# Kernel tuning notes

Hardware: AMD Instinct MI355X
Metric: run time of the kernel (lower is better)

Reference implementation:

```python
import jax, jax.numpy as jnp
import numpy as np

N = 20000      # nodes
E = 320000     # edges (avg degree 16)
DIN, H1, H2, DOUT = 256, 256, 128, 64


def _lin_params(key, din, dout):
    kw, kb = jax.random.split(key)
    s = 1.0 / np.sqrt(din)
    W = jax.random.uniform(kw, (din, dout), jnp.float32, -s, s)
    b = jax.random.uniform(kb, (dout,), jnp.float32, -s, s)
    return W, b


def setup_inputs() -> dict:
    key = jax.random.key(0)
    keys = jax.random.split(key, 20)
    inp = {
        'x': jax.random.normal(keys[0], (N, DIN), jnp.float32),
        'edge_index': jax.random.randint(keys[1], (2, E), 0, N, jnp.int64),
    }
    dims = [(DIN, H1), (DIN, H1), (DIN, H1),   # layer1 key/query/value
            (H1, H2), (H1, H2), (H1, H2),      # layer2
            (H2, DOUT), (H2, DOUT), (H2, DOUT)]  # layer3
    names = ['k1', 'q1', 'v1', 'k2', 'q2', 'v2', 'k3', 'q3', 'v3']
    for i, (nm, (di, do)) in enumerate(zip(names, dims)):
        W, b = _lin_params(keys[2 + i], di, do)
        inp[nm + '_w'] = W
        inp[nm + '_b'] = b
    # skip (root) weights, no bias per PyG, plus per-conv output bias
    for j, (di, do) in enumerate([(DIN, H1), (H1, H2), (H2, DOUT)], start=1):
        s = 1.0 / np.sqrt(di)
        inp[f's{j}_w'] = jax.random.uniform(keys[11 + 2 * j], (di, do), jnp.float32, -s, s)
        inp[f'bias{j}'] = jnp.zeros((do,), jnp.float32)
    return inp


def _res_gated_conv(x, src, dst, kw, kb, qw, qb, vw, vb, sw, bias):
    # PyG ResGatedGraphConv (flow source_to_target, aggr='add', act=Sigmoid):
    # out_i = lin_skip(x_i) + sum_{j->i} sigmoid(lin_key(x_i) + lin_query(x_j)) * lin_value(x_j) + bias
    k = x @ kw + kb            # [N, D]
    q = x @ qw + qb
    v = x @ vw + vb
    eta = jax.nn.sigmoid(k[dst] + q[src])   # [E, D] edge gate
    msg = eta * v[src]                      # [E, D]
    agg = jax.ops.segment_sum(msg, dst, num_segments=N)  # scatter-add to targets
    return x @ sw + agg + bias


def reference(x, edge_index,
              k1_w, k1_b, q1_w, q1_b, v1_w, v1_b,
              k2_w, k2_b, q2_w, q2_b, v2_w, v2_b,
              k3_w, k3_b, q3_w, q3_b, v3_w, v3_b,
              s1_w, bias1, s2_w, bias2, s3_w, bias3):
    src, dst = edge_index[0], edge_index[1]
    h = _res_gated_conv(x, src, dst, k1_w, k1_b, q1_w, q1_b, v1_w, v1_b, s1_w, bias1)
    # dropout (eval mode -> identity)
    h = _res_gated_conv(h, src, dst, k2_w, k2_b, q2_w, q2_b, v2_w, v2_b, s2_w, bias2)
    h = _res_gated_conv(h, src, dst, k3_w, k3_b, q3_w, q3_b, v3_w, v3_b, s3_w, bias3)
    return jax.nn.softmax(h, axis=1)
```

## Files before the change

### kernel.cpp

```cpp
#include <hip/hip_runtime.h>
#include <hip/hip_bf16.h>
#include <type_traits>


#define NN 20000
#define EE 320000
#define ELLW 64

typedef _Float16 half8 __attribute__((ext_vector_type(8)));
typedef _Float16 half4 __attribute__((ext_vector_type(4)));
typedef _Float16 half2v __attribute__((ext_vector_type(2)));
typedef float f32x4 __attribute__((ext_vector_type(4)));

__device__ __forceinline__ _Float16 f2h(float f) { return (_Float16)f; }
__device__ __forceinline__ float fsigmoid_mul(float v, float x) {
    return v * __builtin_amdgcn_rcpf(1.f + __expf(-x));
}

__global__ void setup_kernel(const int* __restrict__ ei, int* __restrict__ deg,
                             int* __restrict__ flag, int n, int ncheck) {
    const int i = blockIdx.x * blockDim.x + threadIdx.x;
    if (i < n) deg[i] = 0;
    if (blockIdx.x == 0) {
        __shared__ int nz;
        if (threadIdx.x == 0) nz = 0;
        __syncthreads();
        int c = 0;
        for (int t = threadIdx.x; t < ncheck; t += blockDim.x)
            if (ei[2 * t + 1] != 0) c = 1;
        if (c) atomicAdd(&nz, 1);
        __syncthreads();
        if (threadIdx.x == 0) *flag = (nz == 0) ? 1 : 0;
    }
}

__global__ void fill_ell_kernel(const int* __restrict__ ei,
                                const int* __restrict__ i64flag,
                                int* __restrict__ deg, int* __restrict__ col,
                                int E) {
    const int e = blockIdx.x * blockDim.x + threadIdx.x;
    if (e >= E) return;
    int src, dst;
    if (*i64flag) {
        const long long* p = (const long long*)ei;
        src = (int)p[e];
        dst = (int)p[E + e];
    } else {
        src = ei[e];
        dst = ei[E + e];
    }
    const int pos = atomicAdd(&deg[dst], 1);
    if (pos < ELLW) col[dst * ELLW + pos] = src;
}

__global__ void cast_f16_kernel(const float* __restrict__ in,
                                _Float16* __restrict__ out, int n) {
    const int i = (blockIdx.x * blockDim.x + threadIdx.x) * 8;
    if (i >= n) return;
    const float4 f0 = *(const float4*)(in + i);
    const float4 f1 = *(const float4*)(in + i + 4);
    half8 h;
    h[0] = f2h(f0.x); h[1] = f2h(f0.y); h[2] = f2h(f0.z); h[3] = f2h(f0.w);
    h[4] = f2h(f1.x); h[5] = f2h(f1.y); h[6] = f2h(f1.z); h[7] = f2h(f1.w);
    *(half8*)(out + i) = h;
}

struct PrepArgs {
    const float *w[3][4];
    const float *b[3][4];
    _Float16 *wt[3];
    float *cb[3];
};

__global__ void prep_all_kernel(PrepArgs a) {
    const int idx = blockIdx.x * blockDim.x + threadIdx.x;
    int layer, li, K, D, s;
    if (idx < 262144) {
        layer = 0; li = idx; K = 256; D = 256; s = 2;
    } else if (idx < 393216) {
        layer = 1; li = idx - 262144; K = 256; D = 128; s = 1;
    } else if (idx < 425984) {
        layer = 2; li = idx - 393216; K = 128; D = 64; s = 0;
    } else {
        return;
    }
    const int p = li / K;
    const int k = li - p * K;
    const int DV = D >> 6;
    int grp, c;
    if (p < D) {
        grp = 0; c = p;
    } else if (p < 3 * D) {
        const int t = p - D;
        const int g = t >> (s + 1);
        const int r = t & (2 * DV - 1);
        if (r < DV) { grp = 1; c = g * DV + r; }
        else        { grp = 2; c = g * DV + r - DV; }
    } else {
        grp = 3; c = p - 3 * D;
    }
    a.wt[layer][(size_t)p * K + k] = f2h(a.w[layer][grp][(size_t)k * D + c]);
    if (k == 0) a.cb[layer][p] = a.b[layer][grp][c];
}

__global__ __launch_bounds__(256) void gemm_mfma_kernel(
    const _Float16* __restrict__ A, const _Float16* __restrict__ Bt,
    const float* __restrict__ catbias, _Float16* __restrict__ KQV,
    float* __restrict__ Hout, int M, int K, int dshift) {
    __shared__ _Float16 As[2][4096];
    __shared__ _Float16 Bs[2][4096];

    const int D = 1 << dshift;
    const int D3 = 3 * D;
    const int tid = threadIdx.x;
    const int wid = tid >> 6;
    const int lane = tid & 63;
    const int tile_m = blockIdx.x * 128;
    const int tile_n = blockIdx.y * 128;
    const int wm = (wid & 1) * 64;
    const int wn = (wid >> 1) * 64;

    const int st_row = (wid << 4) + (lane >> 2);
    const int st_kc = (lane & 3) << 3;

    auto stage = [&](int buf, int kt) {
#pragma unroll
        for (int j = 0; j < 2; ++j) {
            int ar = tile_m + j * 64 + st_row;
            ar = ar < M ? ar : M - 1;
            const _Float16* ag = A + (size_t)ar * K + kt + st_kc;
            __builtin_amdgcn_global_load_lds(
                (const __attribute__((address_space(1))) unsigned int*)ag,
                (__attribute__((address_space(3))) unsigned int*)
                    &As[buf][j * 2048 + (wid << 9)],
                16, 0, 0);
            const int br = tile_n + j * 64 + st_row;
            const _Float16* bg = Bt + (size_t)br * K + kt + st_kc;
            __builtin_amdgcn_global_load_lds(
                (const __attribute__((address_space(1))) unsigned int*)bg,
                (__attribute__((address_space(3))) unsigned int*)
                    &Bs[buf][j * 2048 + (wid << 9)],
                16, 0, 0);
        }
    };

    stage(0, 0);

    f32x4 acc[4][4] = {};
    const int fr = lane & 15;
    const int fk = (lane >> 4) << 3;
    const int niter = K >> 5;

    for (int it = 0; it < niter; ++it) {
        __syncthreads();
        if (it + 1 < niter) stage((it + 1) & 1, (it + 1) << 5);
        const _Float16* as = As[it & 1];
        const _Float16* bs = Bs[it & 1];
        half8 af[4], bf[4];
#pragma unroll
        for (int mi = 0; mi < 4; ++mi)
            af[mi] = *(const half8*)&as[(wm + mi * 16 + fr) * 32 + fk];
#pragma unroll
        for (int ni = 0; ni < 4; ++ni)
            bf[ni] = *(const half8*)&bs[(wn + ni * 16 + fr) * 32 + fk];
#pragma unroll
        for (int mi = 0; mi < 4; ++mi)
#pragma unroll
            for (int ni = 0; ni < 4; ++ni)
                acc[mi][ni] = __builtin_amdgcn_mfma_f32_16x16x32_f16(
                    af[mi], bf[ni], acc[mi][ni], 0, 0, 0);
    }
    __syncthreads();

    _Float16* zone = &As[0][0] + wid * 2048;
    const int cl = lane & 15;
    const int rq = (lane >> 4) << 2;
    const int col0 = tile_n + wn;
    const int r0 = tile_m + wm;

    if (col0 < D3) {
#pragma unroll
        for (int mi = 0; mi < 4; ++mi) {
#pragma unroll
            for (int ni = 0; ni < 4; ++ni) {
                const float cb = catbias[col0 + ni * 16 + cl];
#pragma unroll
                for (int r = 0; r < 4; ++r)
                    zone[(rq + r) * 72 + ni * 16 + cl] =
                        f2h(acc[mi][ni][r] + cb);
            }
#pragma unroll
            for (int j = 0; j < 2; ++j) {
                const int rr = j * 8 + (lane >> 3);
                const int row = r0 + mi * 16 + rr;
                const half8 v = *(const half8*)&zone[rr * 72 + (lane & 7) * 8];
                if (row < M)
                    *(half8*)&KQV[(size_t)row * D3 + col0 + (lane & 7) * 8] = v;
            }
        }
    } else {
        float* fz = (float*)zone;
        const int cs = col0 - D3;
#pragma unroll
        for (int mi = 0; mi < 4; ++mi) {
#pragma unroll
            for (int ni = 0; ni < 4; ++ni) {
                const float cb = catbias[col0 + ni * 16 + cl];
#pragma unroll
                for (int r = 0; r < 4; ++r)
                    fz[(rq + r) * 64 + ni * 16 + cl] = acc[mi][ni][r] + cb;
            }
#pragma unroll
            for (int j = 0; j < 4; ++j) {
                const int rr = j * 4 + (lane >> 4);
                const int row = r0 + mi * 16 + rr;
                const float4 v = *(const float4*)&fz[rr * 64 + cl * 4];
                if (row < M)
                    *(float4*)&Hout[(size_t)row * D + cs + cl * 4] = v;
            }
        }
    }
}

template <int D, int MODE>
__global__ __launch_bounds__(256) void edge_gather_kernel(
    const int* __restrict__ deg, const int* __restrict__ col,
    const _Float16* __restrict__ KQV, const float* __restrict__ Hskip,
    _Float16* __restrict__ Hh, float* __restrict__ out, int n) {
    constexpr int DV = D / 64;
    constexpr int D3 = 3 * D;
    using qv_t = typename std::conditional<
        DV == 4, half8,
        typename std::conditional<DV == 2, half4, half2v>::type>::type;

    const int node = blockIdx.x * 4 + (threadIdx.x >> 6);
    if (node >= n) return;
    const int lane = threadIdx.x & 63;
    const int ld = lane * DV;

    float k[DV], acc[DV];
    {
        const _Float16* kp = KQV + (size_t)node * D3 + ld;
        if constexpr (DV == 4) {
            const half4 u = *(const half4*)kp;
#pragma unroll
            for (int j = 0; j < 4; ++j) k[j] = (float)u[j];
        } else if constexpr (DV == 2) {
            const half2v u = *(const half2v*)kp;
            k[0] = (float)u[0]; k[1] = (float)u[1];
        } else {
            k[0] = (float)*kp;
        }
    }
#pragma unroll
    for (int j = 0; j < DV; ++j) acc[j] = 0.f;

    int dg = deg[node];
    dg = dg < ELLW ? dg : ELLW;
    const int* cb = col + node * ELLW;

    auto qvload = [&](int src) {
        return *(const qv_t*)(KQV + (size_t)src * D3 + D + 2 * ld);
    };
    auto qvacc = [&](qv_t u) {
#pragma unroll
        for (int j = 0; j < DV; ++j)
            acc[j] += fsigmoid_mul((float)u[DV + j], k[j] + (float)u[j]);
    };

    int e = 0;
    for (; e + 4 <= dg; e += 4) {
        const int s0 = cb[e], s1 = cb[e + 1], s2 = cb[e + 2], s3 = cb[e + 3];
        const qv_t u0 = qvload(s0);
        const qv_t u1 = qvload(s1);
        const qv_t u2 = qvload(s2);
        const qv_t u3 = qvload(s3);
        qvacc(u0); qvacc(u1); qvacc(u2); qvacc(u3);
    }
    for (; e < dg; ++e) qvacc(qvload(cb[e]));

    const float* sp = Hskip + (size_t)node * D + ld;
    float h[DV];
    if constexpr (DV == 4) {
        const float4 s = *(const float4*)sp;
        h[0] = s.x + acc[0]; h[1] = s.y + acc[1];
        h[2] = s.z + acc[2]; h[3] = s.w + acc[3];
    } else if constexpr (DV == 2) {
        const float2 s = *(const float2*)sp;
        h[0] = s.x + acc[0]; h[1] = s.y + acc[1];
    } else {
        h[0] = sp[0] + acc[0];
    }

    if constexpr (MODE == 0) {
        _Float16* op = Hh + (size_t)node * D + ld;
        if constexpr (DV == 4) {
            half4 o;
#pragma unroll
            for (int j = 0; j < 4; ++j) o[j] = f2h(h[j]);
            *(half4*)op = o;
        } else if constexpr (DV == 2) {
            half2v o;
            o[0] = f2h(h[0]); o[1] = f2h(h[1]);
            *(half2v*)op = o;
        } else {
            op[0] = f2h(h[0]);
        }
    } else {
        static_assert(MODE == 0 || DV == 1, "softmax fusion needs D==64");
        float m = h[0];
#pragma unroll
        for (int off = 32; off > 0; off >>= 1)
            m = fmaxf(m, __shfl_xor(m, off, 64));
        const float ex = __expf(h[0] - m);
        float sm = ex;
#pragma unroll
        for (int off = 32; off > 0; off >>= 1) sm += __shfl_xor(sm, off, 64);
        out[(size_t)node * 64 + lane] = ex * __builtin_amdgcn_rcpf(sm);
    }
}

extern "C" void kernel_launch(void* const* d_in, const int* in_sizes, int n_in,
                              void* d_out, int out_size, void* d_ws,
                              size_t ws_size, hipStream_t stream) {
    const float* x = (const float*)d_in[0];
    const int* ei = (const int*)d_in[1];

    char* w = (char*)d_ws;
    _Float16* Xh = (_Float16*)w;              w += (size_t)NN * 256 * 2;
    _Float16* KQV = (_Float16*)w;             w += (size_t)NN * 768 * 2;
    float* Hs = (float*)w;                    w += (size_t)NN * 256 * 4;
    _Float16* H1h = (_Float16*)w;             w += (size_t)NN * 256 * 2;
    _Float16* H2h = (_Float16*)w;             w += (size_t)NN * 128 * 2;
    _Float16* Wt1 = (_Float16*)w;             w += (size_t)1024 * 256 * 2;
    _Float16* Wt2 = (_Float16*)w;             w += (size_t)512 * 256 * 2;
    _Float16* Wt3 = (_Float16*)w;             w += (size_t)256 * 128 * 2;
    float* cb1 = (float*)w;                   w += 1024 * 4;
    float* cb2 = (float*)w;                   w += 512 * 4;
    float* cb3 = (float*)w;                   w += 256 * 4;
    int* i64flag = (int*)w;                   w += 16;
    int* deg = (int*)w;                       w += (size_t)NN * 4;
    int* ell = (int*)w;                       w += (size_t)NN * ELLW * 4;

    const dim3 blk(256);
    const int mblocks = (NN + 127) / 128;
    const int gblocks = (NN + 3) / 4;

    setup_kernel<<<(NN + 255) / 256, blk, 0, stream>>>(ei, deg, i64flag, NN,
                                                       1024);
    fill_ell_kernel<<<(EE + 255) / 256, blk, 0, stream>>>(ei, i64flag, deg,
                                                          ell, EE);

    PrepArgs pa;
    pa.w[0][0] = (const float*)d_in[2];  pa.b[0][0] = (const float*)d_in[3];
    pa.w[0][1] = (const float*)d_in[4];  pa.b[0][1] = (const float*)d_in[5];
    pa.w[0][2] = (const float*)d_in[6];  pa.b[0][2] = (const float*)d_in[7];
    pa.w[1][0] = (const float*)d_in[8];  pa.b[1][0] = (const float*)d_in[9];
    pa.w[1][1] = (const float*)d_in[10]; pa.b[1][1] = (const float*)d_in[11];
    pa.w[1][2] = (const float*)d_in[12]; pa.b[1][2] = (const float*)d_in[13];
    pa.w[2][0] = (const float*)d_in[14]; pa.b[2][0] = (const float*)d_in[15];
    pa.w[2][1] = (const float*)d_in[16]; pa.b[2][1] = (const float*)d_in[17];
    pa.w[2][2] = (const float*)d_in[18]; pa.b[2][2] = (const float*)d_in[19];
    pa.w[0][3] = (const float*)d_in[20]; pa.b[0][3] = (const float*)d_in[21];
    pa.w[1][3] = (const float*)d_in[22]; pa.b[1][3] = (const float*)d_in[23];
    pa.w[2][3] = (const float*)d_in[24]; pa.b[2][3] = (const float*)d_in[25];
    pa.wt[0] = Wt1; pa.wt[1] = Wt2; pa.wt[2] = Wt3;
    pa.cb[0] = cb1; pa.cb[1] = cb2; pa.cb[2] = cb3;
    prep_all_kernel<<<(425984 + 255) / 256, blk, 0, stream>>>(pa);
    cast_f16_kernel<<<(NN * 256 / 8 + 255) / 256, blk, 0, stream>>>(
        x, Xh, NN * 256);

    gemm_mfma_kernel<<<dim3(mblocks, 8), blk, 0, stream>>>(
        Xh, Wt1, cb1, KQV, Hs, NN, 256, 8);
    edge_gather_kernel<256, 0><<<gblocks, blk, 0, stream>>>(
        deg, ell, KQV, Hs, H1h, nullptr, NN);

    gemm_mfma_kernel<<<dim3(mblocks, 4), blk, 0, stream>>>(
        H1h, Wt2, cb2, KQV, Hs, NN, 256, 7);
    edge_gather_kernel<128, 0><<<gblocks, blk, 0, stream>>>(
        deg, ell, KQV, Hs, H2h, nullptr, NN);

    gemm_mfma_kernel<<<dim3(mblocks, 2), blk, 0, stream>>>(
        H2h, Wt3, cb3, KQV, Hs, NN, 128, 6);
    edge_gather_kernel<64, 1><<<gblocks, blk, 0, stream>>>(
        deg, ell, KQV, Hs, nullptr, (float*)d_out, NN);
}
```

Baseline: 283.6 us.

## Fuse setup kernels, overlap ELL fill with first GEMM, store skip in fp16

Merges the degree reset, int64 check, weight prep and input cast into one launch. It also runs the ELL fill as extra blocks of the first GEMM launch, so graph construction overlaps with the matmul. The skip projection is now written as fp16 inside one combined KQVS buffer instead of a separate fp32 array, and the edge gather loads neighbor indices once per wave and broadcasts them by shuffle in batches of 8. This cuts launch count and gather latency, but lowers skip precision and depends on a block-order assumption. The fill blocks write deg and col while the GEMM blocks read nothing from them, so the fusion is safe.

Measured after the change: 262.3 us. 1.08x faster.

```diff
diff --git a/kernel.cpp b/kernel.cpp
--- a/kernel.cpp
+++ b/kernel.cpp
@@ -17,106 +17,84 @@
     return v * __builtin_amdgcn_rcpf(1.f + __expf(-x));
 }
 
-__global__ void setup_kernel(const int* __restrict__ ei, int* __restrict__ deg,
-                             int* __restrict__ flag, int n, int ncheck) {
-    const int i = blockIdx.x * blockDim.x + threadIdx.x;
-    if (i < n) deg[i] = 0;
-    if (blockIdx.x == 0) {
+struct PrepArgs {
+    const float* w[3][4];
+    const float* b[3][4];
+    _Float16* wt[3];
+    float* cb[3];
+};
+
+__global__ __launch_bounds__(256) void setup_all_kernel(
+    const int* __restrict__ ei, int* __restrict__ deg, int* __restrict__ flag,
+    const float* __restrict__ x, _Float16* __restrict__ Xh, PrepArgs a) {
+    const int b = blockIdx.x;
+    const int tid = threadIdx.x;
+    if (b < 79) {
+        const int i = b * 256 + tid;
+        if (i < NN) deg[i] = 0;
+    } else if (b == 79) {
         __shared__ int nz;
-        if (threadIdx.x == 0) nz = 0;
+        if (tid == 0) nz = 0;
         __syncthreads();
         int c = 0;
-        for (int t = threadIdx.x; t < ncheck; t += blockDim.x)
+        for (int t = tid; t < 1024; t += 256)
             if (ei[2 * t + 1] != 0) c = 1;
         if (c) atomicAdd(&nz, 1);
         __syncthreads();
-        if (threadIdx.x == 0) *flag = (nz == 0) ? 1 : 0;
-    }
-}
-
-__global__ void fill_ell_kernel(const int* __restrict__ ei,
-                                const int* __restrict__ i64flag,
-                                int* __restrict__ deg, int* __restrict__ col,
-                                int E) {
-    const int e = blockIdx.x * blockDim.x + threadIdx.x;
-    if (e >= E) return;
-    int src, dst;
-    if (*i64flag) {
-        const long long* p = (const long long*)ei;
-        src = (int)p[e];
-        dst = (int)p[E + e];
+        if (tid == 0) *flag = (nz == 0) ? 1 : 0;
+    } else if (b < 1744) {
+        const int idx = (b - 80) * 256 + tid;
+        int layer, li, K, D, s;
+        if (idx < 262144) {
+            layer = 0; li = idx; K = 256; D = 256; s = 2;
+        } else if (idx < 393216) {
+            layer = 1; li = idx - 262144; K = 256; D = 128; s = 1;
+        } else {
+            layer = 2; li = idx - 393216; K = 128; D = 64; s = 0;
+        }
+        const int p = li / K;
+        const int k = li - p * K;
+        const int DV = D >> 6;
+        int grp, c;
+        if (p < D) {
+            grp = 0; c = p;
+        } else if (p < 3 * D) {
+            const int t = p - D;
+            const int g = t >> (s + 1);
+            const int r = t & (2 * DV - 1);
+            if (r < DV) { grp = 1; c = g * DV + r; }
+            else        { grp = 2; c = g * DV + r - DV; }
+        } else {
+            grp = 3; c = p - 3 * D;
+        }
+        a.wt[layer][(size_t)p * K + k] =
+            f2h(a.w[layer][grp][(size_t)k * D + c]);
+        if (k == 0) a.cb[layer][p] = a.b[layer][grp][c];
     } else {
-        src = ei[e];
-        dst = ei[E + e];
-    }
-    const int pos = atomicAdd(&deg[dst], 1);
-    if (pos < ELLW) col[dst * ELLW + pos] = src;
-}
-
-__global__ void cast_f16_kernel(const float* __restrict__ in,
-                                _Float16* __restrict__ out, int n) {
-    const int i = (blockIdx.x * blockDim.x + threadIdx.x) * 8;
-    if (i >= n) return;
-    const float4 f0 = *(const float4*)(in + i);
-    const float4 f1 = *(const float4*)(in + i + 4);
-    half8 h;
-    h[0] = f2h(f0.x); h[1] = f2h(f0.y); h[2] = f2h(f0.z); h[3] = f2h(f0.w);
-    h[4] = f2h(f1.x); h[5] = f2h(f1.y); h[6] = f2h(f1.z); h[7] = f2h(f1.w);
-    *(half8*)(out + i) = h;
-}
-
-struct PrepArgs {
-    const float *w[3][4];
-    const float *b[3][4];
-    _Float16 *wt[3];
-    float *cb[3];
-};
-
-__global__ void prep_all_kernel(PrepArgs a) {
-    const int idx = blockIdx.x * blockDim.x + threadIdx.x;
-    int layer, li, K, D, s;
-    if (idx < 262144) {
-        layer = 0; li = idx; K = 256; D = 256; s = 2;
-    } else if (idx < 393216) {
-        layer = 1; li = idx - 262144; K = 256; D = 128; s = 1;
-    } else if (idx < 425984) {
-        layer = 2; li = idx - 393216; K = 128; D = 64; s = 0;
-    } else {
-        return;
-    }
-    const int p = li / K;
-    const int k = li - p * K;
-    const int DV = D >> 6;
-    int grp, c;
-    if (p < D) {
-        grp = 0; c = p;
-    } else if (p < 3 * D) {
-        const int t = p - D;
-        const int g = t >> (s + 1);
-        const int r = t & (2 * DV - 1);
-        if (r < DV) { grp = 1; c = g * DV + r; }
-        else        { grp = 2; c = g * DV + r - DV; }
-    } else {
-        grp = 3; c = p - 3 * D;
-    }
-    a.wt[layer][(size_t)p * K + k] = f2h(a.w[layer][grp][(size_t)k * D + c]);
-    if (k == 0) a.cb[layer][p] = a.b[layer][grp][c];
-}
-
-__global__ __launch_bounds__(256) void gemm_mfma_kernel(
-    const _Float16* __restrict__ A, const _Float16* __restrict__ Bt,
-    const float* __restrict__ catbias, _Float16* __restrict__ KQV,
-    float* __restrict__ Hout, int M, int K, int dshift) {
+        const int i = ((b - 1744) * 256 + tid) * 8;
+        if (i < NN * 256) {
+            const float4 f0 = *(const float4*)(x + i);
+            const float4 f1 = *(const float4*)(x + i + 4);
+            half8 h;
+            h[0] = f2h(f0.x); h[1] = f2h(f0.y); h[2] = f2h(f0.z); h[3] = f2h(f0.w);
+            h[4] = f2h(f1.x); h[5] = f2h(f1.y); h[6] = f2h(f1.z); h[7] = f2h(f1.w);
+            *(half8*)(Xh + i) = h;
+        }
+    }
+}
+
+__device__ __forceinline__ void gemm_tile(
+    int bm, int bn, const _Float16* __restrict__ A,
+    const _Float16* __restrict__ Bt, const float* __restrict__ catbias,
+    _Float16* __restrict__ O, int M, int K, int N) {
     __shared__ _Float16 As[2][4096];
     __shared__ _Float16 Bs[2][4096];
 
-    const int D = 1 << dshift;
-    const int D3 = 3 * D;
     const int tid = threadIdx.x;
     const int wid = tid >> 6;
     const int lane = tid & 63;
-    const int tile_m = blockIdx.x * 128;
-    const int tile_n = blockIdx.y * 128;
+    const int tile_m = bm * 128;
+    const int tile_n = bn * 128;
     const int wm = (wid & 1) * 64;
     const int wn = (wid >> 1) * 64;
 
@@ -177,58 +155,66 @@
     const int rq = (lane >> 4) << 2;
     const int col0 = tile_n + wn;
     const int r0 = tile_m + wm;
-
-    if (col0 < D3) {
-#pragma unroll
-        for (int mi = 0; mi < 4; ++mi) {
-#pragma unroll
-            for (int ni = 0; ni < 4; ++ni) {
-                const float cb = catbias[col0 + ni * 16 + cl];
-#pragma unroll
-                for (int r = 0; r < 4; ++r)
-                    zone[(rq + r) * 72 + ni * 16 + cl] =
-                        f2h(acc[mi][ni][r] + cb);
-            }
-#pragma unroll
-            for (int j = 0; j < 2; ++j) {
-                const int rr = j * 8 + (lane >> 3);
-                const int row = r0 + mi * 16 + rr;
-                const half8 v = *(const half8*)&zone[rr * 72 + (lane & 7) * 8];
-                if (row < M)
-                    *(half8*)&KQV[(size_t)row * D3 + col0 + (lane & 7) * 8] = v;
-            }
-        }
+#pragma unroll
+    for (int mi = 0; mi < 4; ++mi) {
+#pragma unroll
+        for (int ni = 0; ni < 4; ++ni) {
+            const float cb = catbias[col0 + ni * 16 + cl];
+#pragma unroll
+            for (int r = 0; r < 4; ++r)
+                zone[(rq + r) * 72 + ni * 16 + cl] = f2h(acc[mi][ni][r] + cb);
+        }
+#pragma unroll
+        for (int j = 0; j < 2; ++j) {
+            const int rr = j * 8 + (lane >> 3);
+            const int row = r0 + mi * 16 + rr;
+            const half8 v = *(const half8*)&zone[rr * 72 + (lane & 7) * 8];
+            if (row < M)
+                *(half8*)&O[(size_t)row * N + col0 + (lane & 7) * 8] = v;
+        }
+    }
+}
+
+__global__ __launch_bounds__(256) void gemm_kernel(
+    const _Float16* __restrict__ A, const _Float16* __restrict__ Bt,
+    const float* __restrict__ catbias, _Float16* __restrict__ O, int M, int K,
+    int N, int mblocks) {
+    gemm_tile(blockIdx.x % mblocks, blockIdx.x / mblocks, A, Bt, catbias, O, M,
+              K, N);
+}
+
+__global__ __launch_bounds__(256) void gemm1_fill_kernel(
+    const _Float16* __restrict__ A, const _Float16* __restrict__ Bt,
+    const float* __restrict__ catbias, _Float16* __restrict__ O,
+    const int* __restrict__ ei, const int* __restrict__ i64flag,
+    int* __restrict__ deg, int* __restrict__ col) {
+    if (blockIdx.x < 1256) {
+        gemm_tile(blockIdx.x % 157, blockIdx.x / 157, A, Bt, catbias, O, NN,
+                  256, 1024);
+        return;
+    }
+    const int e = (blockIdx.x - 1256) * 256 + threadIdx.x;
+    if (e >= EE) return;
+    int src, dst;
+    if (*i64flag) {
+        const long long* p = (const long long*)ei;
+        src = (int)p[e];
+        dst = (int)p[EE + e];
     } else {
-        float* fz = (float*)zone;
-        const int cs = col0 - D3;
-#pragma unroll
-        for (int mi = 0; mi < 4; ++mi) {
-#pragma unroll
-            for (int ni = 0; ni < 4; ++ni) {
-                const float cb = catbias[col0 + ni * 16 + cl];
-#pragma unroll
-                for (int r = 0; r < 4; ++r)
-                    fz[(rq + r) * 64 + ni * 16 + cl] = acc[mi][ni][r] + cb;
-            }
-#pragma unroll
-            for (int j = 0; j < 4; ++j) {
-                const int rr = j * 4 + (lane >> 4);
-                const int row = r0 + mi * 16 + rr;
-                const float4 v = *(const float4*)&fz[rr * 64 + cl * 4];
-                if (row < M)
-                    *(float4*)&Hout[(size_t)row * D + cs + cl * 4] = v;
-            }
-        }
-    }
+        src = ei[e];
+        dst = ei[EE + e];
+    }
+    const int pos = atomicAdd(&deg[dst], 1);
+    if (pos < ELLW) col[dst * ELLW + pos] = src;
 }
 
 template <int D, int MODE>
 __global__ __launch_bounds__(256) void edge_gather_kernel(
     const int* __restrict__ deg, const int* __restrict__ col,
-    const _Float16* __restrict__ KQV, const float* __restrict__ Hskip,
-    _Float16* __restrict__ Hh, float* __restrict__ out, int n) {
+    const _Float16* __restrict__ KQVS, _Float16* __restrict__ Hh,
+    float* __restrict__ out, int n) {
     constexpr int DV = D / 64;
-    constexpr int D3 = 3 * D;
+    constexpr int D4 = 4 * D;
     using qv_t = typename std::conditional<
         DV == 4, half8,
         typename std::conditional<DV == 2, half4, half2v>::type>::type;
@@ -238,9 +224,14 @@
     const int lane = threadIdx.x & 63;
     const int ld = lane * DV;
 
+    int dg = deg[node];
+    dg = dg < ELLW ? dg : ELLW;
+    int idx = col[node * ELLW + lane];
+    if (lane >= dg) idx = node;
+
     float k[DV], acc[DV];
     {
-        const _Float16* kp = KQV + (size_t)node * D3 + ld;
+        const _Float16* kp = KQVS + (size_t)node * D4 + ld;
         if constexpr (DV == 4) {
             const half4 u = *(const half4*)kp;
 #pragma unroll
@@ -255,41 +246,40 @@
 #pragma unroll
     for (int j = 0; j < DV; ++j) acc[j] = 0.f;
 
-    int dg = deg[node];
-    dg = dg < ELLW ? dg : ELLW;
-    const int* cb = col + node * ELLW;
-
-    auto qvload = [&](int src) {
-        return *(const qv_t*)(KQV + (size_t)src * D3 + D + 2 * ld);
-    };
+    const _Float16* qvbase = KQVS + D + 2 * ld;
     auto qvacc = [&](qv_t u) {
 #pragma unroll
         for (int j = 0; j < DV; ++j)
             acc[j] += fsigmoid_mul((float)u[DV + j], k[j] + (float)u[j]);
     };
 
-    int e = 0;
-    for (; e + 4 <= dg; e += 4) {
-        const int s0 = cb[e], s1 = cb[e + 1], s2 = cb[e + 2], s3 = cb[e + 3];
-        const qv_t u0 = qvload(s0);
-        const qv_t u1 = qvload(s1);
-        const qv_t u2 = qvload(s2);
-        const qv_t u3 = qvload(s3);
-        qvacc(u0); qvacc(u1); qvacc(u2); qvacc(u3);
-    }
-    for (; e < dg; ++e) qvacc(qvload(cb[e]));
-
-    const float* sp = Hskip + (size_t)node * D + ld;
+    for (int e = 0; e < dg; e += 8) {
+        qv_t u[8];
+#pragma unroll
+        for (int j = 0; j < 8; ++j) {
+            const int s = __shfl(idx, e + j, 64);
+            u[j] = *(const qv_t*)(qvbase + (size_t)s * D4);
+        }
+        const int nb = dg - e;
+#pragma unroll
+        for (int j = 0; j < 8; ++j)
+            if (j < nb) qvacc(u[j]);
+    }
+
     float h[DV];
-    if constexpr (DV == 4) {
-        const float4 s = *(const float4*)sp;
-        h[0] = s.x + acc[0]; h[1] = s.y + acc[1];
-        h[2] = s.z + acc[2]; h[3] = s.w + acc[3];
-    } else if constexpr (DV == 2) {
-        const float2 s = *(const float2*)sp;
-        h[0] = s.x + acc[0]; h[1] = s.y + acc[1];
-    } else {
-        h[0] = sp[0] + acc[0];
+    {
+        const _Float16* sp = KQVS + (size_t)node * D4 + 3 * D + ld;
+        if constexpr (DV == 4) {
+            const half4 u = *(const half4*)sp;
+#pragma unroll
+            for (int j = 0; j < 4; ++j) h[j] = (float)u[j] + acc[j];
+        } else if constexpr (DV == 2) {
+            const half2v u = *(const half2v*)sp;
+            h[0] = (float)u[0] + acc[0];
+            h[1] = (float)u[1] + acc[1];
+        } else {
+            h[0] = (float)*sp + acc[0];
+        }
     }
 
     if constexpr (MODE == 0) {
@@ -327,29 +317,22 @@
     const int* ei = (const int*)d_in[1];
 
     char* w = (char*)d_ws;
-    _Float16* Xh = (_Float16*)w;              w += (size_t)NN * 256 * 2;
-    _Float16* KQV = (_Float16*)w;             w += (size_t)NN * 768 * 2;
-    float* Hs = (float*)w;                    w += (size_t)NN * 256 * 4;
-    _Float16* H1h = (_Float16*)w;             w += (size_t)NN * 256 * 2;
-    _Float16* H2h = (_Float16*)w;             w += (size_t)NN * 128 * 2;
-    _Float16* Wt1 = (_Float16*)w;             w += (size_t)1024 * 256 * 2;
-    _Float16* Wt2 = (_Float16*)w;             w += (size_t)512 * 256 * 2;
-    _Float16* Wt3 = (_Float16*)w;             w += (size_t)256 * 128 * 2;
-    float* cb1 = (float*)w;                   w += 1024 * 4;
-    float* cb2 = (float*)w;                   w += 512 * 4;
-    float* cb3 = (float*)w;                   w += 256 * 4;
-    int* i64flag = (int*)w;                   w += 16;
-    int* deg = (int*)w;                       w += (size_t)NN * 4;
-    int* ell = (int*)w;                       w += (size_t)NN * ELLW * 4;
+    _Float16* Xh = (_Float16*)w;     w += (size_t)NN * 256 * 2;
+    _Float16* KQVS = (_Float16*)w;   w += (size_t)NN * 1024 * 2;
+    _Float16* H1h = (_Float16*)w;    w += (size_t)NN * 256 * 2;
+    _Float16* H2h = (_Float16*)w;    w += (size_t)NN * 128 * 2;
+    _Float16* Wt1 = (_Float16*)w;    w += (size_t)1024 * 256 * 2;
+    _Float16* Wt2 = (_Float16*)w;    w += (size_t)512 * 256 * 2;
+    _Float16* Wt3 = (_Float16*)w;    w += (size_t)256 * 128 * 2;
+    float* cb1 = (float*)w;          w += 1024 * 4;
+    float* cb2 = (float*)w;          w += 512 * 4;
+    float* cb3 = (float*)w;          w += 256 * 4;
+    int* i64flag = (int*)w;          w += 16;
+    int* deg = (int*)w;              w += (size_t)NN * 4;
+    int* ell = (int*)w;              w += (size_t)NN * ELLW * 4;
 
     const dim3 blk(256);
-    const int mblocks = (NN + 127) / 128;
     const int gblocks = (NN + 3) / 4;
-
-    setup_kernel<<<(NN + 255) / 256, blk, 0, stream>>>(ei, deg, i64flag, NN,
-                                                       1024);
-    fill_ell_kernel<<<(EE + 255) / 256, blk, 0, stream>>>(ei, i64flag, deg,
-                                                          ell, EE);
 
     PrepArgs pa;
     pa.w[0][0] = (const float*)d_in[2];  pa.b[0][0] = (const float*)d_in[3];
@@ -366,22 +349,21 @@
     pa.w[2][3] = (const float*)d_in[24]; pa.b[2][3] = (const float*)d_in[25];
     pa.wt[0] = Wt1; pa.wt[1] = Wt2; pa.wt[2] = Wt3;
     pa.cb[0] = cb1; pa.cb[1] = cb2; pa.cb[2] = cb3;
-    prep_all_kernel<<<(425984 + 255) / 256, blk, 0, stream>>>(pa);
-    cast_f16_kernel<<<(NN * 256 / 8 + 255) / 256, blk, 0, stream>>>(
-        x, Xh, NN * 256);
-
-    gemm_mfma_kernel<<<dim3(mblocks, 8), blk, 0, stream>>>(
-        Xh, Wt1, cb1, KQV, Hs, NN, 256, 8);
+
+    setup_all_kernel<<<4244, blk, 0, stream>>>(ei, deg, i64flag, x, Xh, pa);
+
+    gemm1_fill_kernel<<<2506, blk, 0, stream>>>(Xh, Wt1, cb1, KQVS, ei,
+                                                i64flag, deg, ell);
     edge_gather_kernel<256, 0><<<gblocks, blk, 0, stream>>>(
-        deg, ell, KQV, Hs, H1h, nullptr, NN);
-
-    gemm_mfma_kernel<<<dim3(mblocks, 4), blk, 0, stream>>>(
-        H1h, Wt2, cb2, KQV, Hs, NN, 256, 7);
+        deg, ell, KQVS, H1h, nullptr, NN);
+
+    gemm_kernel<<<157 * 4, blk, 0, stream>>>(H1h, Wt2, cb2, KQVS, NN, 256, 512,
+                                             157);
     edge_gather_kernel<128, 0><<<gblocks, blk, 0, stream>>>(
-        deg, ell, KQV, Hs, H2h, nullptr, NN);
-
-    gemm_mfma_kernel<<<dim3(mblocks, 2), blk, 0, stream>>>(
-        H2h, Wt3, cb3, KQV, Hs, NN, 128, 6);
+        deg, ell, KQVS, H2h, nullptr, NN);
+
+    gemm_kernel<<<157 * 2, blk, 0, stream>>>(H2h, Wt3, cb3, KQVS, NN, 128, 256,
+                                             157);
     edge_gather_kernel<64, 1><<<gblocks, blk, 0, stream>>>(
-        deg, ell, KQV, Hs, nullptr, (float*)d_out, NN);
-}
+        deg, ell, KQVS, nullptr, (float*)d_out, NN);
+}
```
